# Performance work log

Measured on AMD Instinct MI355X. Metric: run time of the kernel, lower is better.

The kernel has to match this reference:

```python
import jax, jax.numpy as jnp
import numpy as np

EPS = 1e-5

def layer_norm(x, w, b):
    m = jnp.mean(x, axis=-1, keepdims=True)
    v = jnp.mean(jnp.square(x - m), axis=-1, keepdims=True)
    return (x - m) * jax.lax.rsqrt(v + EPS) * w + b

def setup_inputs() -> dict:
    key = jax.random.key(0)
    B, S, D, H = 4, 2048, 768, 12
    Dh, F = D // H, 4 * D
    ks = jax.random.split(key, 16)
    s = 0.02
    return {
        "x":    jax.random.normal(ks[0], (B, S, D), dtype=jnp.float32),
        # per-head q/k/v projections stacked over heads: [H, D, Dh]
        "Wq":   jax.random.normal(ks[1], (H, D, Dh), dtype=jnp.float32) * s,
        "bq":   jnp.zeros((H, Dh), dtype=jnp.float32),
        "Wk":   jax.random.normal(ks[2], (H, D, Dh), dtype=jnp.float32) * s,
        "bk":   jnp.zeros((H, Dh), dtype=jnp.float32),
        "Wv":   jax.random.normal(ks[3], (H, D, Dh), dtype=jnp.float32) * s,
        "bv":   jnp.zeros((H, Dh), dtype=jnp.float32),
        "Wo":   jax.random.normal(ks[4], (D, D), dtype=jnp.float32) * s,
        "bo":   jnp.zeros((D,), dtype=jnp.float32),
        "W1":   jax.random.normal(ks[5], (D, F), dtype=jnp.float32) * s,
        "b1":   jnp.zeros((F,), dtype=jnp.float32),
        "W2":   jax.random.normal(ks[6], (F, D), dtype=jnp.float32) * s,
        "b2":   jnp.zeros((D,), dtype=jnp.float32),
        "ln1_w": jnp.ones((D,), dtype=jnp.float32),
        "ln1_b": jnp.zeros((D,), dtype=jnp.float32),
        "ln2_w": jnp.ones((D,), dtype=jnp.float32),
        "ln2_b": jnp.zeros((D,), dtype=jnp.float32),
    }

def reference(x, Wq, bq, Wk, bk, Wv, bv, Wo, bo, W1, b1, W2, b2,
              ln1_w, ln1_b, ln2_w, ln2_b):
    B, S, D = x.shape
    H, _, Dh = Wq.shape
    scale = jnp.sqrt(jnp.float32(Dh))  # torch scales by sqrt(dout)
    # q,k,v: [B, H, S, Dh]
    q = jnp.einsum('bsd,hde->bhse', x, Wq) + bq[None, :, None, :]
    k = jnp.einsum('bsd,hde->bhse', x, Wk) + bk[None, :, None, :]
    v = jnp.einsum('bsd,hde->bhse', x, Wv) + bv[None, :, None, :]
    scores = jnp.einsum('bhqe,bhke->bhqk', q, k) / scale  # [B,H,S,S]
    causal = jnp.tril(jnp.ones((S, S), dtype=bool))
    scores = jnp.where(causal[None, None], scores, -jnp.inf)
    attn = jax.nn.softmax(scores, axis=-1)
    ctx = jnp.einsum('bhqk,bhke->bhqe', attn, v)           # [B,H,S,Dh]
    ctx = jnp.transpose(ctx, (0, 2, 1, 3)).reshape(B, S, D)  # concat heads
    att_out = ctx @ Wo + bo
    h = layer_norm(x + att_out, ln1_w, ln1_b)  # post-norm, dropout=0
    ff = jax.nn.gelu(h @ W1 + b1, approximate=False) @ W2 + b2
    return layer_norm(h + ff, ln2_w, ln2_b)
```

## Files before the change

### kernel.cpp

```cpp
#include <hip/hip_runtime.h>
#include <hip/hip_bf16.h>
#include <math.h>

#define B_ 4
#define S_ 2048
#define D_ 768
#define H_ 12
#define DH_ 64
#define F_ 3072
#define NTOK (B_*S_)
#define BH_ (B_*H_)

typedef __hip_bfloat16 bf16;
typedef __attribute__((ext_vector_type(8))) short bf16x8;
typedef __attribute__((ext_vector_type(4))) float f32x4;
typedef __attribute__((ext_vector_type(4))) _Float16 half4;
typedef __attribute__((ext_vector_type(8))) _Float16 half8;

#define GLD16(g, l) __builtin_amdgcn_global_load_lds( \
    (__attribute__((address_space(1))) void*)(uintptr_t)(g), \
    (__attribute__((address_space(3))) void*)(uintptr_t)(l), 16, 0, 0)

__device__ __forceinline__ float bs2f(short s){
  union { unsigned int u; float f; } cv; cv.u = ((unsigned int)(unsigned short)s) << 16; return cv.f;
}
__device__ __forceinline__ float b2f(bf16 v){ return __bfloat162float(v); }
__device__ __forceinline__ bf16 f2b(float v){ return __float2bfloat16(v); }
__device__ __forceinline__ short f2bb(float v){ bf16 b = f2b(v); short s; __builtin_memcpy(&s, &b, 2); return s; }

__device__ __forceinline__ void wgbar(){
  __builtin_amdgcn_s_barrier();
  asm volatile("" ::: "memory");
}

__device__ __forceinline__ float gelu_fast(float v){
  const float c0 = -2.302208157f;
  const float c1 = -0.102943238f;
  float w = v*v;
  float z = v * __builtin_fmaf(c1, w, c0);
  float t = __builtin_amdgcn_exp2f(z);
  return v * __builtin_amdgcn_rcpf(1.0f + t);
}

__global__ void f32_to_bf16_k(const float4* __restrict__ in, short4* __restrict__ out, int n4){
  int i = blockIdx.x*256 + threadIdx.x;
  if (i < n4){
    float4 v = in[i];
    short4 o;
    o.x = f2bb(v.x); o.y = f2bb(v.y); o.z = f2bb(v.z); o.w = f2bb(v.w);
    out[i] = o;
  }
}

__global__ __launch_bounds__(256) void transpose_f32_bf16_k(const float* __restrict__ in,
    bf16* __restrict__ out, int K, int N){
  __shared__ float t[32][33];
  const int kb = blockIdx.y*32, nb = blockIdx.x*32;
  const int x = threadIdx.x & 31, y = threadIdx.x >> 5;
#pragma unroll
  for (int yy = y; yy < 32; yy += 8)
    t[yy][x] = in[(size_t)(kb+yy)*N + nb + x];
  __syncthreads();
#pragma unroll
  for (int yy = y; yy < 32; yy += 8)
    out[(size_t)(nb+yy)*K + kb + x] = f2b(t[x][yy]);
}

__global__ void pack_qkv_t_k(const float* __restrict__ Wq, const float* __restrict__ bq,
                             const float* __restrict__ Wk, const float* __restrict__ bk,
                             const float* __restrict__ Wv, const float* __restrict__ bv,
                             bf16* __restrict__ Wt, float* __restrict__ bcat){
  int idx = blockIdx.x*256 + threadIdx.x;
  if (idx < 3*D_*D_){
    int n = idx / D_;
    int k = idx - n*D_;
    int which = n / D_;
    int cc = n - which*D_;
    int h = cc >> 6, e = cc & 63;
    const float* W = (which==0) ? Wq : ((which==1) ? Wk : Wv);
    Wt[idx] = f2b(W[((size_t)h*D_ + k)*DH_ + e]);
  }
  if (idx < 3*D_){
    int which = idx / D_;
    int cc = idx - which*D_;
    int h = cc >> 6, e = cc & 63;
    const float* bb = (which==0) ? bq : ((which==1) ? bk : bv);
    bcat[idx] = bb[h*DH_ + e];
  }
}

#define STAGE_A(bufi_, kh_, kt_) do { \
    GLD16(gA  + (size_t)(kt_)*64 + (kh_)*32, asb + ((bufi_)<<15) + ((kh_)<<14)); \
    GLD16(gA2 + (size_t)(kt_)*64 + (kh_)*32, asb + ((bufi_)<<15) + ((kh_)<<14) + 8192); } while(0)
#define STAGE_B(bufi_, kh_, kt_) do { \
    GLD16(gB  + (size_t)(kt_)*64 + (kh_)*32, bsb + ((bufi_)<<15) + ((kh_)<<14)); \
    GLD16(gB2 + (size_t)(kt_)*64 + (kh_)*32, bsb + ((bufi_)<<15) + ((kh_)<<14) + 8192); } while(0)
#define AFRAG(bufi_, ks_, i_) (*(const bf16x8*)(AsB + ((bufi_)<<15) + ((ks_)<<14) + ((wm + (i_)*16 + l16)<<6) + fsw))
#define BFRAG(bufi_, ks_, j_) (*(const bf16x8*)(BsB + ((bufi_)<<15) + ((ks_)<<14) + ((wn + (j_)*16 + l16)<<6) + fsw))

template<int EPI>
__global__ __launch_bounds__(512, 2) void mgemm256_k(
    const bf16* __restrict__ A, const bf16* __restrict__ Bt,
    const float* __restrict__ bias, bf16* __restrict__ C,
    int M, int N, int K,
    bf16* __restrict__ qb, bf16* __restrict__ kbuf, _Float16* __restrict__ vt)
{
  __shared__ __align__(16) bf16 As[32768];
  __shared__ __align__(16) bf16 Bs[32768];
  const int tid  = threadIdx.x;
  const int wave = tid >> 6, lane = tid & 63;
  const int quad = lane >> 4, l16 = lane & 15;
  const int wm = (wave >> 2) * 128;
  const int wn = (wave & 3) * 64;

  const int NX = gridDim.x;
  const int f  = blockIdx.y * NX + blockIdx.x;
  const int xcd = f & 7;
  const int j0  = f >> 3;
  const int bx  = j0 % NX;
  const int by  = (j0 / NX) * 8 + xcd;
  const int m0 = by * 256, n0 = bx * 256;

  const int srow = tid >> 2;
  const int sg   = (tid & 3) ^ ((tid >> 3) & 3);
  const bf16* gA  = A  + (size_t)(m0 + srow)*K + sg*8;
  const bf16* gA2 = A  + (size_t)(m0 + 128 + srow)*K + sg*8;
  const bf16* gB  = Bt + (size_t)(n0 + srow)*K + sg*8;
  const bf16* gB2 = Bt + (size_t)(n0 + 128 + srow)*K + sg*8;
  const uintptr_t asb = (uintptr_t)(void*)As + (size_t)wave*1024;
  const uintptr_t bsb = (uintptr_t)(void*)Bs + (size_t)wave*1024;

  const char* AsB = (const char*)As;
  const char* BsB = (const char*)Bs;
  const int fsw = (quad ^ ((l16 >> 1) & 3)) * 16;

  f32x4 acc[8][4];
#pragma unroll
  for (int i=0;i<8;i++)
#pragma unroll
    for (int j2=0;j2<4;j2++) acc[i][j2] = (f32x4)0.f;

  const int KT = K >> 6;

  STAGE_A(0, 0, 0); STAGE_B(0, 0, 0); STAGE_A(0, 1, 0); STAGE_B(0, 1, 0);
  asm volatile("s_waitcnt vmcnt(4)" ::: "memory");
  wgbar();

  for (int kt = 0; kt < KT; ++kt){
    const int bufc = kt & 1, bufn = bufc ^ 1;
    const bool pf = (kt + 1) < KT;
    bf16x8 af[4], bfr[4];

#pragma unroll
    for (int i=0;i<4;i++) af[i] = AFRAG(bufc, 0, i);
#pragma unroll
    for (int j2=0;j2<4;j2++) bfr[j2] = BFRAG(bufc, 0, j2);
    if (pf) STAGE_A(bufn, 0, kt+1);
    wgbar();
    __builtin_amdgcn_s_setprio(1);
#pragma unroll
    for (int i=0;i<4;i++)
#pragma unroll
      for (int j2=0;j2<4;j2++)
        acc[i][j2] = __builtin_amdgcn_mfma_f32_16x16x32_bf16(af[i], bfr[j2], acc[i][j2], 0, 0, 0);
    __builtin_amdgcn_s_setprio(0);
    wgbar();

#pragma unroll
    for (int i=0;i<4;i++) af[i] = AFRAG(bufc, 0, 4+i);
    if (pf) STAGE_B(bufn, 0, kt+1);
    wgbar();
    __builtin_amdgcn_s_setprio(1);
#pragma unroll
    for (int i=0;i<4;i++)
#pragma unroll
      for (int j2=0;j2<4;j2++)
        acc[4+i][j2] = __builtin_amdgcn_mfma_f32_16x16x32_bf16(af[i], bfr[j2], acc[4+i][j2], 0, 0, 0);
    __builtin_amdgcn_s_setprio(0);
    if (pf) asm volatile("s_waitcnt vmcnt(4)" ::: "memory");
    else    asm volatile("s_waitcnt vmcnt(0)" ::: "memory");
    wgbar();

#pragma unroll
    for (int i=0;i<4;i++) af[i] = AFRAG(bufc, 1, i);
#pragma unroll
    for (int j2=0;j2<4;j2++) bfr[j2] = BFRAG(bufc, 1, j2);
    if (pf) STAGE_A(bufn, 1, kt+1);
    wgbar();
    __builtin_amdgcn_s_setprio(1);
#pragma unroll
    for (int i=0;i<4;i++)
#pragma unroll
      for (int j2=0;j2<4;j2++)
        acc[i][j2] = __builtin_amdgcn_mfma_f32_16x16x32_bf16(af[i], bfr[j2], acc[i][j2], 0, 0, 0);
    __builtin_amdgcn_s_setprio(0);
    wgbar();

#pragma unroll
    for (int i=0;i<4;i++) af[i] = AFRAG(bufc, 1, 4+i);
    if (pf) STAGE_B(bufn, 1, kt+1);
    wgbar();
    __builtin_amdgcn_s_setprio(1);
#pragma unroll
    for (int i=0;i<4;i++)
#pragma unroll
      for (int j2=0;j2<4;j2++)
        acc[4+i][j2] = __builtin_amdgcn_mfma_f32_16x16x32_bf16(af[i], bfr[j2], acc[4+i][j2], 0, 0, 0);
    __builtin_amdgcn_s_setprio(0);
    if (pf) asm volatile("s_waitcnt vmcnt(4)" ::: "memory");
    wgbar();
  }

#pragma unroll
  for (int i=0;i<8;i++){
#pragma unroll
    for (int j2=0;j2<4;j2++){
      const int n = n0 + wn + j2*16 + l16;
      const int m_base = m0 + wm + i*16 + quad*4;
      if (EPI == 0){
        const int which = n / D_;
        const int cc = n - which*D_;
        const int h = cc >> 6, e = cc & 63;
        if (which == 2){
          const int b = m_base >> 11, s = m_base & (S_-1);
          const int sl = s & 63;
          const int perm = ((sl>>2)&3)*16 + ((sl>>4)&3)*4;
          half4 hv;
#pragma unroll
          for (int r=0;r<4;r++) hv[r] = (_Float16)(acc[i][j2][r] + bias[n]);
          *(half4*)(vt + ((size_t)(b*H_+h)*DH_ + e)*S_ + (s & ~63) + perm) = hv;
        } else {
          bf16* dst = (which==0) ? qb : kbuf;
          const float sc2 = (which==0) ? 0.18033688f : 1.0f;
#pragma unroll
          for (int r=0;r<4;r++){
            const int m = m_base + r;
            const int b = m >> 11, s = m & (S_-1);
            dst[((size_t)(b*H_+h)*S_ + s)*DH_ + e] = f2b((acc[i][j2][r] + bias[n]) * sc2);
          }
        }
      } else {
#pragma unroll
        for (int r=0;r<4;r++){
          const int m = m_base + r;
          float v = acc[i][j2][r] + bias[n];
          C[(size_t)m*N + n] = f2b(gelu_fast(v));
        }
      }
    }
  }
}
#undef STAGE_A
#undef STAGE_B
#undef AFRAG
#undef BFRAG

__global__ __launch_bounds__(256) void mgemm64_k(
    const bf16* __restrict__ A, const bf16* __restrict__ Bt,
    const float* __restrict__ bias, const bf16* __restrict__ aux,
    bf16* __restrict__ C, int M, int N, int K)
{
  __shared__ bf16 As[8192];
  __shared__ bf16 Bs[16384];
  const int tid  = threadIdx.x;
  const int wave = tid >> 6, lane = tid & 63;
  const int quad = lane >> 4, l16 = lane & 15;
  const int wm = (wave >> 1) * 32, wn = (wave & 1) * 64;

  const int NX = gridDim.x;
  const int f  = blockIdx.y * NX + blockIdx.x;
  const int xcd = f & 7;
  const int j   = f >> 3;
  const int bx  = j % NX;
  const int by  = (j / NX) * 8 + xcd;
  const int m0 = by * 64, n0 = bx * 128;

  const int srow8 = lane >> 3;
  const int g     = (lane & 7) ^ srow8;
  const bf16* gA0 = A  + (size_t)(m0 + wave*16 +      srow8)*K + g*8;
  const bf16* gA1 = A  + (size_t)(m0 + wave*16 +  8 + srow8)*K + g*8;
  const bf16* gB0 = Bt + (size_t)(n0 + wave*32 +      srow8)*K + g*8;
  const bf16* gB1 = Bt + (size_t)(n0 + wave*32 +  8 + srow8)*K + g*8;
  const bf16* gB2 = Bt + (size_t)(n0 + wave*32 + 16 + srow8)*K + g*8;
  const bf16* gB3 = Bt + (size_t)(n0 + wave*32 + 24 + srow8)*K + g*8;
  const uintptr_t asb = (uintptr_t)(void*)As + (size_t)wave*16*128;
  const uintptr_t bsb = (uintptr_t)(void*)Bs + (size_t)wave*32*128;

  f32x4 acc[2][4];
#pragma unroll
  for (int i=0;i<2;i++)
#pragma unroll
    for (int j2=0;j2<4;j2++) acc[i][j2] = (f32x4)0.f;

  const char* AsB = (const char*)As;
  const char* BsB = (const char*)Bs;
  const int KT = K >> 6;

  GLD16(gA0, asb);
  GLD16(gA1, asb + 1024);
  GLD16(gB0, bsb);
  GLD16(gB1, bsb + 1024);
  GLD16(gB2, bsb + 2048);
  GLD16(gB3, bsb + 3072);
  gA0 += 64; gA1 += 64; gB0 += 64; gB1 += 64; gB2 += 64; gB3 += 64;
  asm volatile("s_waitcnt vmcnt(0)" ::: "memory");
  wgbar();

  for (int kt = 0; kt < KT; ++kt){
    const int cur = kt & 1, nxt = cur ^ 1;
    const bool pf = (kt + 1) < KT;
    if (pf){
      const uintptr_t ao = asb + nxt*8192;
      const uintptr_t bo = bsb + nxt*16384;
      GLD16(gA0, ao);
      GLD16(gA1, ao + 1024);
      GLD16(gB0, bo);
      GLD16(gB1, bo + 1024);
      GLD16(gB2, bo + 2048);
      GLD16(gB3, bo + 3072);
      gA0 += 64; gA1 += 64; gB0 += 64; gB1 += 64; gB2 += 64; gB3 += 64;
    }
    const char* Ac = AsB + cur*8192;
    const char* Bc = BsB + cur*16384;
#pragma unroll
    for (int kq = 0; kq < 2; kq++){
      const int cbase = kq*4 + quad;
      bf16x8 af[2], bfr[4];
#pragma unroll
      for (int i=0;i<2;i++){
        const int m = wm + i*16 + l16;
        af[i] = *(const bf16x8*)(Ac + (m << 7) + ((cbase ^ (m & 7)) << 4));
      }
#pragma unroll
      for (int j2=0;j2<4;j2++){
        const int n = wn + j2*16 + l16;
        bfr[j2] = *(const bf16x8*)(Bc + (n << 7) + ((cbase ^ (n & 7)) << 4));
      }
#pragma unroll
      for (int i=0;i<2;i++)
#pragma unroll
        for (int j2=0;j2<4;j2++)
          acc[i][j2] = __builtin_amdgcn_mfma_f32_16x16x32_bf16(af[i], bfr[j2], acc[i][j2], 0, 0, 0);
    }
    if (pf) asm volatile("s_waitcnt vmcnt(0)" ::: "memory");
    wgbar();
  }

#pragma unroll
  for (int i=0;i<2;i++){
#pragma unroll
    for (int j2=0;j2<4;j2++){
      const int n = n0 + wn + j2*16 + l16;
      const int m_base = m0 + wm + i*16 + quad*4;
#pragma unroll
      for (int r=0;r<4;r++){
        const int m = m_base + r;
        float v = acc[i][j2][r] + bias[n] + b2f(aux[(size_t)m*N + n]);
        C[(size_t)m*N + n] = f2b(v);
      }
    }
  }
}

__global__ __launch_bounds__(256) void fattn_k(const bf16* __restrict__ qb,
    const bf16* __restrict__ kb, const _Float16* __restrict__ vt, bf16* __restrict__ ctx)
{
  __shared__ __align__(16) char smem[19456];
  bf16     (*Ks)[72] = (bf16(*)[72])smem;
  _Float16 (*Vs)[72] = (_Float16(*)[72])(smem + 9216);
  float* maxb  = (float*)(smem + 18432);
  float* libuf = (float*)(smem + 18944);
  float* Obuf  = (float*)smem;

  const int bh = blockIdx.x;
  const int qt = 31 - blockIdx.y;
  const int q0 = qt * 64;
  const int tid = threadIdx.x;
  const int wave = tid >> 6, lane = tid & 63;
  const int quad = lane >> 4, l16 = lane & 15;
  const int kh = wave >> 1, qh = wave & 1;
  const size_t kbase = (size_t)bh * S_ * DH_;

  bf16x8 qf[2][2];
#pragma unroll
  for (int nf=0; nf<2; nf++)
#pragma unroll
    for (int h=0; h<2; h++)
      qf[nf][h] = *(const bf16x8*)(qb + kbase + (size_t)(q0 + qh*32 + nf*16 + l16)*DH_ + h*32 + quad*8);

  f32x4 o[4][2];
#pragma unroll
  for (int df=0; df<4; df++){ o[df][0] = (f32x4)0.f; o[df][1] = (f32x4)0.f; }
  float mi[2] = {-1e30f, -1e30f}, li[2] = {0.f, 0.f};

  for (int kt = 0; kt <= qt; ++kt){
    const int k0 = kt * 64;
    __syncthreads();
    {
      const int r = tid >> 2, seg = (tid & 3) * 16;
      const bf16* ksrc = kb + kbase + (size_t)(k0 + r)*DH_ + seg;
      bf16x8 ka = *(const bf16x8*)ksrc;
      bf16x8 kc2 = *(const bf16x8*)(ksrc + 8);
      *(bf16x8*)&Ks[r][seg]   = ka;
      *(bf16x8*)&Ks[r][seg+8] = kc2;
      const _Float16* vsrc = vt + ((size_t)bh*DH_ + r)*S_ + k0 + seg;
      half8 va = *(const half8*)vsrc;
      half8 vb2 = *(const half8*)(vsrc + 8);
      *(half8*)&Vs[r][seg]   = va;
      *(half8*)&Vs[r][seg+8] = vb2;
    }
    __syncthreads();

    bf16x8 af[2][2];
#pragma unroll
    for (int mf=0; mf<2; mf++)
#pragma unroll
      for (int h=0; h<2; h++)
        af[mf][h] = *(const bf16x8*)&Ks[kh*32 + mf*16 + l16][h*32 + quad*8];
    f32x4 sc[2][2];
#pragma unroll
    for (int mf=0; mf<2; mf++)
#pragma unroll
      for (int nf=0; nf<2; nf++){
        f32x4 t = __builtin_amdgcn_mfma_f32_16x16x32_bf16(af[mf][0], qf[nf][0], (f32x4)0.f, 0, 0, 0);
        sc[mf][nf] = __builtin_amdgcn_mfma_f32_16x16x32_bf16(af[mf][1], qf[nf][1], t, 0, 0, 0);
      }

    if (kt == qt){
#pragma unroll
      for (int mf=0; mf<2; mf++){
        const int keyl = kh*32 + mf*16 + quad*4;
#pragma unroll
        for (int nf=0; nf<2; nf++){
          const int ql = qh*32 + nf*16 + l16;
#pragma unroll
          for (int r=0; r<4; r++)
            if (keyl + r > ql) sc[mf][nf][r] = -1e30f;
        }
      }
    }

    float mw[2];
#pragma unroll
    for (int nf=0; nf<2; nf++){
      float mx = -1e30f;
#pragma unroll
      for (int mf=0; mf<2; mf++)
#pragma unroll
        for (int r=0; r<4; r++) mx = fmaxf(mx, sc[mf][nf][r]);
      mx = fmaxf(mx, __shfl_xor(mx, 16));
      mx = fmaxf(mx, __shfl_xor(mx, 32));
      mw[nf] = mx;
    }
    if (quad == 0){
      maxb[kh*64 + qh*32 + l16]      = mw[0];
      maxb[kh*64 + qh*32 + 16 + l16] = mw[1];
    }
    __syncthreads();

    const float tm0 = fmaxf(mw[0], maxb[(1-kh)*64 + qh*32 + l16]);
    const float tm1 = fmaxf(mw[1], maxb[(1-kh)*64 + qh*32 + 16 + l16]);
    const bool need = !__all((tm0 - mi[0] <= 8.f) && (tm1 - mi[1] <= 8.f));
    if (need){
      const float mn0 = fmaxf(mi[0], tm0);
      const float mn1 = fmaxf(mi[1], tm1);
      const float a0 = __builtin_amdgcn_exp2f(mi[0] - mn0);
      const float a1 = __builtin_amdgcn_exp2f(mi[1] - mn1);
      mi[0] = mn0; mi[1] = mn1;
      li[0] *= a0; li[1] *= a1;
#pragma unroll
      for (int df=0; df<4; df++)
#pragma unroll
        for (int r=0; r<4; r++){ o[df][0][r] *= a0; o[df][1][r] *= a1; }
    }

    half4 pf[2][2];
#pragma unroll
    for (int nf=0; nf<2; nf++){
      float rs = 0.f;
#pragma unroll
      for (int mf=0; mf<2; mf++)
#pragma unroll
        for (int r=0; r<4; r++){
          float p = __builtin_amdgcn_exp2f(sc[mf][nf][r] - mi[nf]);
          pf[mf][nf][r] = (_Float16)p;
          rs += p;
        }
      rs += __shfl_xor(rs, 16);
      rs += __shfl_xor(rs, 32);
      li[nf] += rs;
    }

#pragma unroll
    for (int df=0; df<4; df++){
      half8 vv = *(const half8*)&Vs[df*16 + l16][quad*16 + kh*8];
      half4 vlo = __builtin_shufflevector(vv, vv, 0,1,2,3);
      half4 vhi = __builtin_shufflevector(vv, vv, 4,5,6,7);
#pragma unroll
      for (int nf=0; nf<2; nf++){
        o[df][nf] = __builtin_amdgcn_mfma_f32_16x16x16f16(vlo, pf[0][nf], o[df][nf], 0, 0, 0);
        o[df][nf] = __builtin_amdgcn_mfma_f32_16x16x16f16(vhi, pf[1][nf], o[df][nf], 0, 0, 0);
      }
    }
  }

  __syncthreads();
  if (quad == 0){
    libuf[kh*64 + qh*32 + l16]      = li[0];
    libuf[kh*64 + qh*32 + 16 + l16] = li[1];
  }
  if (quad == 1){
    maxb[kh*64 + qh*32 + l16]      = mi[0];
    maxb[kh*64 + qh*32 + 16 + l16] = mi[1];
  }
  if (kh == 1){
#pragma unroll
    for (int df=0; df<4; df++)
#pragma unroll
      for (int nf=0; nf<2; nf++)
#pragma unroll
        for (int r=0; r<4; r++)
          Obuf[(qh*64 + df*16 + quad*4 + r)*33 + nf*16 + l16] = o[df][nf][r];
  }
  __syncthreads();
  if (kh == 0){
    const int b = bh / H_, h = bh - (bh / H_)*H_;
#pragma unroll
    for (int nf=0; nf<2; nf++){
      const int q64 = qh*32 + nf*16 + l16;
      const float inv = 1.0f / (libuf[q64] + libuf[64 + q64]);
      const int qtok = q0 + q64;
#pragma unroll
      for (int df=0; df<4; df++){
        short4 pk;
        float v0 = (o[df][nf][0] + Obuf[(qh*64 + df*16 + quad*4 + 0)*33 + nf*16 + l16]) * inv;
        float v1 = (o[df][nf][1] + Obuf[(qh*64 + df*16 + quad*4 + 1)*33 + nf*16 + l16]) * inv;
        float v2 = (o[df][nf][2] + Obuf[(qh*64 + df*16 + quad*4 + 2)*33 + nf*16 + l16]) * inv;
        float v3 = (o[df][nf][3] + Obuf[(qh*64 + df*16 + quad*4 + 3)*33 + nf*16 + l16]) * inv;
        pk.x = f2bb(v0); pk.y = f2bb(v1); pk.z = f2bb(v2); pk.w = f2bb(v3);
        *(short4*)((short*)ctx + ((size_t)(b*S_ + qtok))*D_ + h*DH_ + df*16 + quad*4) = pk;
      }
    }
  }
}

template<typename T> __device__ __forceinline__ void st4(T* p, size_t idx, float a, float b, float c, float d);
template<> __device__ __forceinline__ void st4<float>(float* p, size_t idx, float a, float b, float c, float d){
  float4 v; v.x=a; v.y=b; v.z=c; v.w=d; *(float4*)(p+idx) = v;
}
template<> __device__ __forceinline__ void st4<bf16>(bf16* p, size_t idx, float a, float b, float c, float d){
  short4 v; v.x=f2bb(a); v.y=f2bb(b); v.z=f2bb(c); v.w=f2bb(d); *(short4*)((short*)p+idx) = v;
}

template<typename OutT>
__global__ __launch_bounds__(192) void layernorm_k(const bf16* __restrict__ X,
    const float* __restrict__ g, const float* __restrict__ bta, OutT* __restrict__ Y)
{
  const int row = blockIdx.x;
  const int tid = threadIdx.x;
  const short4 raw = *(const short4*)((const short*)X + (size_t)row*D_ + tid*4);
  const float v0 = bs2f(raw.x), v1 = bs2f(raw.y), v2 = bs2f(raw.z), v3 = bs2f(raw.w);
  float s  = v0+v1+v2+v3;
  float s2 = v0*v0+v1*v1+v2*v2+v3*v3;
#pragma unroll
  for (int o = 32; o > 0; o >>= 1){ s += __shfl_down(s, o); s2 += __shfl_down(s2, o); }
  __shared__ float rs[3], rq[3];
  const int lane = tid & 63, w = tid >> 6;
  if (lane == 0){ rs[w] = s; rq[w] = s2; }
  __syncthreads();
  s  = rs[0]+rs[1]+rs[2];
  s2 = rq[0]+rq[1]+rq[2];
  const float mean = s * (1.0f/D_);
  const float var  = s2 * (1.0f/D_) - mean*mean;
  const float inv  = rsqrtf(var + 1e-5f);
  const float4 g4 = *(const float4*)(g + tid*4);
  const float4 b4 = *(const float4*)(bta + tid*4);
  st4(Y, (size_t)row*D_ + tid*4,
      (v0-mean)*inv*g4.x + b4.x,
      (v1-mean)*inv*g4.y + b4.y,
      (v2-mean)*inv*g4.z + b4.z,
      (v3-mean)*inv*g4.w + b4.w);
}

extern "C" void kernel_launch(void* const* d_in, const int* in_sizes, int n_in,
                              void* d_out, int out_size, void* d_ws, size_t ws_size,
                              hipStream_t stream)
{
  const float* x   = (const float*)d_in[0];
  const float* Wq  = (const float*)d_in[1];
  const float* bq  = (const float*)d_in[2];
  const float* Wk  = (const float*)d_in[3];
  const float* bk  = (const float*)d_in[4];
  const float* Wv  = (const float*)d_in[5];
  const float* bv  = (const float*)d_in[6];
  const float* Wo  = (const float*)d_in[7];
  const float* bo  = (const float*)d_in[8];
  const float* W1  = (const float*)d_in[9];
  const float* b1  = (const float*)d_in[10];
  const float* W2  = (const float*)d_in[11];
  const float* b2  = (const float*)d_in[12];
  const float* g1  = (const float*)d_in[13];
  const float* be1 = (const float*)d_in[14];
  const float* g2  = (const float*)d_in[15];
  const float* be2 = (const float*)d_in[16];
  float* out = (float*)d_out;

  char* ws = (char*)d_ws;
  size_t off = 0;
  auto alloc = [&](size_t bytes)->char*{
    char* p = ws + off; off = (off + bytes + 255) & ~(size_t)255; return p;
  };
  bf16*  xb    = (bf16*) alloc((size_t)NTOK*D_*2);
  bf16*  WcatT = (bf16*) alloc((size_t)3*D_*D_*2);
  float* bcat  = (float*)alloc((size_t)3*D_*4);
  bf16*  WoT   = (bf16*) alloc((size_t)D_*D_*2);
  bf16*  W1T   = (bf16*) alloc((size_t)F_*D_*2);
  bf16*  W2T   = (bf16*) alloc((size_t)D_*F_*2);
  bf16*  r1    = (bf16*) alloc((size_t)NTOK*F_*2);
  bf16*  qb    = r1;
  bf16*  kb    = r1 + (size_t)NTOK*D_;
  _Float16* vt = (_Float16*)(r1 + (size_t)2*NTOK*D_);
  bf16*  ff1   = r1;
  bf16*  ctxb  = (bf16*) alloc((size_t)NTOK*D_*2);
  bf16*  y1    = (bf16*) alloc((size_t)NTOK*D_*2);
  bf16*  hb    = (bf16*) alloc((size_t)NTOK*D_*2);
  bf16*  y2    = ctxb;

  f32_to_bf16_k<<<(NTOK*D_/4+255)/256, 256, 0, stream>>>(
      (const float4*)x, (short4*)xb, NTOK*D_/4);
  transpose_f32_bf16_k<<<dim3(D_/32, D_/32), 256, 0, stream>>>(Wo, WoT, D_, D_);
  transpose_f32_bf16_k<<<dim3(F_/32, D_/32), 256, 0, stream>>>(W1, W1T, D_, F_);
  transpose_f32_bf16_k<<<dim3(D_/32, F_/32), 256, 0, stream>>>(W2, W2T, F_, D_);
  pack_qkv_t_k<<<(3*D_*D_+255)/256, 256, 0, stream>>>(Wq,bq,Wk,bk,Wv,bv,WcatT,bcat);

  mgemm256_k<0><<<dim3(3*D_/256, NTOK/256), 512, 0, stream>>>(
      xb, WcatT, bcat, nullptr, NTOK, 3*D_, D_, qb, kb, vt);

  fattn_k<<<dim3(BH_, S_/64), 256, 0, stream>>>(qb, kb, vt, ctxb);

  mgemm64_k<<<dim3(D_/128, NTOK/64), 256, 0, stream>>>(
      ctxb, WoT, bo, xb, y1, NTOK, D_, D_);

  layernorm_k<bf16><<<NTOK, 192, 0, stream>>>(y1, g1, be1, hb);

  mgemm256_k<2><<<dim3(F_/256, NTOK/256), 512, 0, stream>>>(
      hb, W1T, b1, ff1, NTOK, F_, D_, nullptr, nullptr, nullptr);

  mgemm64_k<<<dim3(D_/128, NTOK/64), 256, 0, stream>>>(
      ff1, W2T, b2, hb, y2, NTOK, D_, F_);

  layernorm_k<float><<<NTOK, 192, 0, stream>>>(y2, g2, be2, out);
}
```

Measured before the change: 401.3 us.

## Pipeline attention K/V loads through rotating LDS buffers and enlarge output GEMM tiles

The flash-attention kernel now prefetches the next K/V tile into registers and stages it in double/triple-buffered LDS, so each iteration needs one barrier instead of two. Softmax probabilities are packed with cvt_pkrtz. Separately, the Wo and W2 GEMMs move from 64x128 to 128x128 tiles, each wave computing 64x64, to raise data reuse per block. In exchange, LDS per block grows, which may lower occupancy, and the larger GEMM tile halves the grid count for those launches.

```diff
diff --git a/kernel.cpp b/kernel.cpp
--- a/kernel.cpp
+++ b/kernel.cpp
@@ -16,6 +16,7 @@
 typedef __attribute__((ext_vector_type(4))) float f32x4;
 typedef __attribute__((ext_vector_type(4))) _Float16 half4;
 typedef __attribute__((ext_vector_type(8))) _Float16 half8;
+typedef __attribute__((ext_vector_type(2))) __fp16 fp16x2;
 
 #define GLD16(g, l) __builtin_amdgcn_global_load_lds( \
     (__attribute__((address_space(1))) void*)(uintptr_t)(g), \
@@ -28,7 +29,19 @@
 __device__ __forceinline__ bf16 f2b(float v){ return __float2bfloat16(v); }
 __device__ __forceinline__ short f2bb(float v){ bf16 b = f2b(v); short s; __builtin_memcpy(&s, &b, 2); return s; }
 
+__device__ __forceinline__ half4 pk4(float p0, float p1, float p2, float p3){
+  union { fp16x2 v2[2]; half4 v4; } u;
+  u.v2[0] = __builtin_amdgcn_cvt_pkrtz(p0, p1);
+  u.v2[1] = __builtin_amdgcn_cvt_pkrtz(p2, p3);
+  return u.v4;
+}
+
 __device__ __forceinline__ void wgbar(){
+  __builtin_amdgcn_s_barrier();
+  asm volatile("" ::: "memory");
+}
+__device__ __forceinline__ void wgbar_lds(){
+  asm volatile("s_waitcnt lgkmcnt(0)" ::: "memory");
   __builtin_amdgcn_s_barrier();
   asm volatile("" ::: "memory");
 }
@@ -255,17 +268,17 @@
 #undef AFRAG
 #undef BFRAG
 
-__global__ __launch_bounds__(256) void mgemm64_k(
+__global__ __launch_bounds__(256) void mgemm128_k(
     const bf16* __restrict__ A, const bf16* __restrict__ Bt,
     const float* __restrict__ bias, const bf16* __restrict__ aux,
     bf16* __restrict__ C, int M, int N, int K)
 {
-  __shared__ bf16 As[8192];
-  __shared__ bf16 Bs[16384];
+  __shared__ __align__(16) bf16 As[16384];
+  __shared__ __align__(16) bf16 Bs[16384];
   const int tid  = threadIdx.x;
   const int wave = tid >> 6, lane = tid & 63;
   const int quad = lane >> 4, l16 = lane & 15;
-  const int wm = (wave >> 1) * 32, wn = (wave & 1) * 64;
+  const int wm = (wave >> 1) * 64, wn = (wave & 1) * 64;
 
   const int NX = gridDim.x;
   const int f  = blockIdx.y * NX + blockIdx.x;
@@ -273,22 +286,18 @@
   const int j   = f >> 3;
   const int bx  = j % NX;
   const int by  = (j / NX) * 8 + xcd;
-  const int m0 = by * 64, n0 = bx * 128;
+  const int m0 = by * 128, n0 = bx * 128;
 
   const int srow8 = lane >> 3;
   const int g     = (lane & 7) ^ srow8;
-  const bf16* gA0 = A  + (size_t)(m0 + wave*16 +      srow8)*K + g*8;
-  const bf16* gA1 = A  + (size_t)(m0 + wave*16 +  8 + srow8)*K + g*8;
-  const bf16* gB0 = Bt + (size_t)(n0 + wave*32 +      srow8)*K + g*8;
-  const bf16* gB1 = Bt + (size_t)(n0 + wave*32 +  8 + srow8)*K + g*8;
-  const bf16* gB2 = Bt + (size_t)(n0 + wave*32 + 16 + srow8)*K + g*8;
-  const bf16* gB3 = Bt + (size_t)(n0 + wave*32 + 24 + srow8)*K + g*8;
-  const uintptr_t asb = (uintptr_t)(void*)As + (size_t)wave*16*128;
+  const bf16* gA = A  + (size_t)(m0 + wave*32 + srow8)*K + g*8;
+  const bf16* gB = Bt + (size_t)(n0 + wave*32 + srow8)*K + g*8;
+  const uintptr_t asb = (uintptr_t)(void*)As + (size_t)wave*32*128;
   const uintptr_t bsb = (uintptr_t)(void*)Bs + (size_t)wave*32*128;
 
-  f32x4 acc[2][4];
-#pragma unroll
-  for (int i=0;i<2;i++)
+  f32x4 acc[4][4];
+#pragma unroll
+  for (int i=0;i<4;i++)
 #pragma unroll
     for (int j2=0;j2<4;j2++) acc[i][j2] = (f32x4)0.f;
 
@@ -296,13 +305,12 @@
   const char* BsB = (const char*)Bs;
   const int KT = K >> 6;
 
-  GLD16(gA0, asb);
-  GLD16(gA1, asb + 1024);
-  GLD16(gB0, bsb);
-  GLD16(gB1, bsb + 1024);
-  GLD16(gB2, bsb + 2048);
-  GLD16(gB3, bsb + 3072);
-  gA0 += 64; gA1 += 64; gB0 += 64; gB1 += 64; gB2 += 64; gB3 += 64;
+#pragma unroll
+  for (int t=0;t<4;t++){
+    GLD16(gA + (size_t)t*8*K, asb + t*1024);
+    GLD16(gB + (size_t)t*8*K, bsb + t*1024);
+  }
+  gA += 64; gB += 64;
   asm volatile("s_waitcnt vmcnt(0)" ::: "memory");
   wgbar();
 
@@ -310,24 +318,23 @@
     const int cur = kt & 1, nxt = cur ^ 1;
     const bool pf = (kt + 1) < KT;
     if (pf){
-      const uintptr_t ao = asb + nxt*8192;
-      const uintptr_t bo = bsb + nxt*16384;
-      GLD16(gA0, ao);
-      GLD16(gA1, ao + 1024);
-      GLD16(gB0, bo);
-      GLD16(gB1, bo + 1024);
-      GLD16(gB2, bo + 2048);
-      GLD16(gB3, bo + 3072);
-      gA0 += 64; gA1 += 64; gB0 += 64; gB1 += 64; gB2 += 64; gB3 += 64;
-    }
-    const char* Ac = AsB + cur*8192;
-    const char* Bc = BsB + cur*16384;
+      const uintptr_t ao = asb + (size_t)nxt*16384;
+      const uintptr_t bo = bsb + (size_t)nxt*16384;
+#pragma unroll
+      for (int t=0;t<4;t++){
+        GLD16(gA + (size_t)t*8*K, ao + t*1024);
+        GLD16(gB + (size_t)t*8*K, bo + t*1024);
+      }
+      gA += 64; gB += 64;
+    }
+    const char* Ac = AsB + (size_t)cur*16384;
+    const char* Bc = BsB + (size_t)cur*16384;
 #pragma unroll
     for (int kq = 0; kq < 2; kq++){
       const int cbase = kq*4 + quad;
-      bf16x8 af[2], bfr[4];
-#pragma unroll
-      for (int i=0;i<2;i++){
+      bf16x8 af[4], bfr[4];
+#pragma unroll
+      for (int i=0;i<4;i++){
         const int m = wm + i*16 + l16;
         af[i] = *(const bf16x8*)(Ac + (m << 7) + ((cbase ^ (m & 7)) << 4));
       }
@@ -337,7 +344,7 @@
         bfr[j2] = *(const bf16x8*)(Bc + (n << 7) + ((cbase ^ (n & 7)) << 4));
       }
 #pragma unroll
-      for (int i=0;i<2;i++)
+      for (int i=0;i<4;i++)
 #pragma unroll
         for (int j2=0;j2<4;j2++)
           acc[i][j2] = __builtin_amdgcn_mfma_f32_16x16x32_bf16(af[i], bfr[j2], acc[i][j2], 0, 0, 0);
@@ -347,7 +354,7 @@
   }
 
 #pragma unroll
-  for (int i=0;i<2;i++){
+  for (int i=0;i<4;i++){
 #pragma unroll
     for (int j2=0;j2<4;j2++){
       const int n = n0 + wn + j2*16 + l16;
@@ -365,11 +372,16 @@
 __global__ __launch_bounds__(256) void fattn_k(const bf16* __restrict__ qb,
     const bf16* __restrict__ kb, const _Float16* __restrict__ vt, bf16* __restrict__ ctx)
 {
-  __shared__ __align__(16) char smem[19456];
-  bf16     (*Ks)[72] = (bf16(*)[72])smem;
-  _Float16 (*Vs)[72] = (_Float16(*)[72])(smem + 9216);
-  float* maxb  = (float*)(smem + 18432);
-  float* libuf = (float*)(smem + 18944);
+  __shared__ __align__(16) char smem[47616];
+  typedef bf16     KsRow[72];
+  typedef _Float16 VsRow[72];
+  KsRow* kp0 = (KsRow*)(smem);
+  KsRow* kp1 = (KsRow*)(smem + 9216);
+  VsRow* vp0 = (VsRow*)(smem + 18432);
+  VsRow* vp1 = (VsRow*)(smem + 27648);
+  VsRow* vp2 = (VsRow*)(smem + 36864);
+  float* maxb  = (float*)(smem + 46080);
+  float* libuf = (float*)(smem + 47104);
   float* Obuf  = (float*)smem;
 
   const int bh = blockIdx.x;
@@ -380,6 +392,10 @@
   const int quad = lane >> 4, l16 = lane & 15;
   const int kh = wave >> 1, qh = wave & 1;
   const size_t kbase = (size_t)bh * S_ * DH_;
+  const int nt = qt + 1;
+
+  const int sr  = tid >> 2;
+  const int seg = (tid & 3) * 16;
 
   bf16x8 qf[2][2];
 #pragma unroll
@@ -393,30 +409,32 @@
   for (int df=0; df<4; df++){ o[df][0] = (f32x4)0.f; o[df][1] = (f32x4)0.f; }
   float mi[2] = {-1e30f, -1e30f}, li[2] = {0.f, 0.f};
 
-  for (int kt = 0; kt <= qt; ++kt){
-    const int k0 = kt * 64;
-    __syncthreads();
-    {
-      const int r = tid >> 2, seg = (tid & 3) * 16;
-      const bf16* ksrc = kb + kbase + (size_t)(k0 + r)*DH_ + seg;
-      bf16x8 ka = *(const bf16x8*)ksrc;
-      bf16x8 kc2 = *(const bf16x8*)(ksrc + 8);
-      *(bf16x8*)&Ks[r][seg]   = ka;
-      *(bf16x8*)&Ks[r][seg+8] = kc2;
-      const _Float16* vsrc = vt + ((size_t)bh*DH_ + r)*S_ + k0 + seg;
-      half8 va = *(const half8*)vsrc;
-      half8 vb2 = *(const half8*)(vsrc + 8);
-      *(half8*)&Vs[r][seg]   = va;
-      *(half8*)&Vs[r][seg+8] = vb2;
-    }
-    __syncthreads();
-
+  bf16x8 ka0, ka1; half8 va0, va1;
+  {
+    const bf16* ks = kb + kbase + (size_t)sr*DH_ + seg;
+    ka0 = *(const bf16x8*)ks; ka1 = *(const bf16x8*)(ks + 8);
+    const _Float16* vs = vt + ((size_t)bh*DH_ + sr)*S_ + seg;
+    va0 = *(const half8*)vs; va1 = *(const half8*)(vs + 8);
+  }
+  *(bf16x8*)&kp0[sr][seg]   = ka0;
+  *(bf16x8*)&kp0[sr][seg+8] = ka1;
+  *(half8*)&vp0[sr][seg]    = va0;
+  *(half8*)&vp0[sr][seg+8]  = va1;
+  if (nt > 1){
+    const bf16* ks = kb + kbase + (size_t)(64 + sr)*DH_ + seg;
+    ka0 = *(const bf16x8*)ks; ka1 = *(const bf16x8*)(ks + 8);
+    const _Float16* vs = vt + ((size_t)bh*DH_ + sr)*S_ + 64 + seg;
+    va0 = *(const half8*)vs; va1 = *(const half8*)(vs + 8);
+  }
+  wgbar_lds();
+
+  for (int kt = 0; kt < nt; ++kt){
     bf16x8 af[2][2];
 #pragma unroll
     for (int mf=0; mf<2; mf++)
 #pragma unroll
       for (int h=0; h<2; h++)
-        af[mf][h] = *(const bf16x8*)&Ks[kh*32 + mf*16 + l16][h*32 + quad*8];
+        af[mf][h] = *(const bf16x8*)&kp0[kh*32 + mf*16 + l16][h*32 + quad*8];
     f32x4 sc[2][2];
 #pragma unroll
     for (int mf=0; mf<2; mf++)
@@ -452,14 +470,29 @@
       mx = fmaxf(mx, __shfl_xor(mx, 32));
       mw[nf] = mx;
     }
+    float* mb = maxb + (kt & 1)*128;
     if (quad == 0){
-      maxb[kh*64 + qh*32 + l16]      = mw[0];
-      maxb[kh*64 + qh*32 + 16 + l16] = mw[1];
-    }
-    __syncthreads();
-
-    const float tm0 = fmaxf(mw[0], maxb[(1-kh)*64 + qh*32 + l16]);
-    const float tm1 = fmaxf(mw[1], maxb[(1-kh)*64 + qh*32 + 16 + l16]);
+      mb[kh*64 + qh*32 + l16]      = mw[0];
+      mb[kh*64 + qh*32 + 16 + l16] = mw[1];
+    }
+
+    if (kt + 1 < nt){
+      *(bf16x8*)&kp1[sr][seg]   = ka0;
+      *(bf16x8*)&kp1[sr][seg+8] = ka1;
+      *(half8*)&vp1[sr][seg]    = va0;
+      *(half8*)&vp1[sr][seg+8]  = va1;
+      if (kt + 2 < nt){
+        const int k0n = (kt + 2) * 64;
+        const bf16* ks = kb + kbase + (size_t)(k0n + sr)*DH_ + seg;
+        ka0 = *(const bf16x8*)ks; ka1 = *(const bf16x8*)(ks + 8);
+        const _Float16* vs = vt + ((size_t)bh*DH_ + sr)*S_ + k0n + seg;
+        va0 = *(const half8*)vs; va1 = *(const half8*)(vs + 8);
+      }
+    }
+    wgbar_lds();
+
+    const float tm0 = fmaxf(mw[0], mb[(1-kh)*64 + qh*32 + l16]);
+    const float tm1 = fmaxf(mw[1], mb[(1-kh)*64 + qh*32 + 16 + l16]);
     const bool need = !__all((tm0 - mi[0] <= 8.f) && (tm1 - mi[1] <= 8.f));
     if (need){
       const float mn0 = fmaxf(mi[0], tm0);
@@ -474,18 +507,19 @@
         for (int r=0; r<4; r++){ o[df][0][r] *= a0; o[df][1][r] *= a1; }
     }
 
-    half4 pf[2][2];
+    half4 pfr[2][2];
 #pragma unroll
     for (int nf=0; nf<2; nf++){
       float rs = 0.f;
 #pragma unroll
-      for (int mf=0; mf<2; mf++)
-#pragma unroll
-        for (int r=0; r<4; r++){
-          float p = __builtin_amdgcn_exp2f(sc[mf][nf][r] - mi[nf]);
-          pf[mf][nf][r] = (_Float16)p;
-          rs += p;
-        }
+      for (int mf=0; mf<2; mf++){
+        const float p0 = __builtin_amdgcn_exp2f(sc[mf][nf][0] - mi[nf]);
+        const float p1 = __builtin_amdgcn_exp2f(sc[mf][nf][1] - mi[nf]);
+        const float p2 = __builtin_amdgcn_exp2f(sc[mf][nf][2] - mi[nf]);
+        const float p3 = __builtin_amdgcn_exp2f(sc[mf][nf][3] - mi[nf]);
+        rs += (p0 + p1) + (p2 + p3);
+        pfr[mf][nf] = pk4(p0, p1, p2, p3);
+      }
       rs += __shfl_xor(rs, 16);
       rs += __shfl_xor(rs, 32);
       li[nf] += rs;
@@ -493,25 +527,24 @@
 
 #pragma unroll
     for (int df=0; df<4; df++){
-      half8 vv = *(const half8*)&Vs[df*16 + l16][quad*16 + kh*8];
+      half8 vv = *(const half8*)&vp0[df*16 + l16][quad*16 + kh*8];
       half4 vlo = __builtin_shufflevector(vv, vv, 0,1,2,3);
       half4 vhi = __builtin_shufflevector(vv, vv, 4,5,6,7);
 #pragma unroll
       for (int nf=0; nf<2; nf++){
-        o[df][nf] = __builtin_amdgcn_mfma_f32_16x16x16f16(vlo, pf[0][nf], o[df][nf], 0, 0, 0);
-        o[df][nf] = __builtin_amdgcn_mfma_f32_16x16x16f16(vhi, pf[1][nf], o[df][nf], 0, 0, 0);
-      }
-    }
+        o[df][nf] = __builtin_amdgcn_mfma_f32_16x16x16f16(vlo, pfr[0][nf], o[df][nf], 0, 0, 0);
+        o[df][nf] = __builtin_amdgcn_mfma_f32_16x16x16f16(vhi, pfr[1][nf], o[df][nf], 0, 0, 0);
+      }
+    }
+
+    { KsRow* t_ = kp0; kp0 = kp1; kp1 = t_; }
+    { VsRow* t_ = vp0; vp0 = vp1; vp1 = vp2; vp2 = t_; }
   }
 
   __syncthreads();
   if (quad == 0){
     libuf[kh*64 + qh*32 + l16]      = li[0];
     libuf[kh*64 + qh*32 + 16 + l16] = li[1];
-  }
-  if (quad == 1){
-    maxb[kh*64 + qh*32 + l16]      = mi[0];
-    maxb[kh*64 + qh*32 + 16 + l16] = mi[1];
   }
   if (kh == 1){
 #pragma unroll
@@ -638,7 +671,7 @@
 
   fattn_k<<<dim3(BH_, S_/64), 256, 0, stream>>>(qb, kb, vt, ctxb);
 
-  mgemm64_k<<<dim3(D_/128, NTOK/64), 256, 0, stream>>>(
+  mgemm128_k<<<dim3(D_/128, NTOK/128), 256, 0, stream>>>(
       ctxb, WoT, bo, xb, y1, NTOK, D_, D_);
 
   layernorm_k<bf16><<<NTOK, 192, 0, stream>>>(y1, g1, be1, hb);
@@ -646,7 +679,7 @@
   mgemm256_k<2><<<dim3(F_/256, NTOK/256), 512, 0, stream>>>(
       hb, W1T, b1, ff1, NTOK, F_, D_, nullptr, nullptr, nullptr);
 
-  mgemm64_k<<<dim3(D_/128, NTOK/64), 256, 0, stream>>>(
+  mgemm128_k<<<dim3(D_/128, NTOK/128), 256, 0, stream>>>(
       ff1, W2T, b2, hb, y2, NTOK, D_, F_);
 
   layernorm_k<float><<<NTOK, 192, 0, stream>>>(y2, g2, be2, out);
```

New measurement: 398.1 us. Within noise of the previous version (-0.8%).
